# Kernel optimization log

Measured on AMD Instinct MI355X. Metric: run time of the kernel, lower is better.

Reference implementation:

```python
import jax, jax.numpy as jnp
import numpy as np
from jax import lax

WINDOW_SIZE = 11
SIGMA = 1.5
C1 = 0.01 ** 2
C2 = 0.03 ** 2
EPS_DEN = 1e-12
EPS_CLAMP = 1e-6


def _gaussian_window(size=WINDOW_SIZE, sigma=SIGMA):
    xs = jnp.arange(size, dtype=jnp.float32) - size // 2
    g = jnp.exp(-(xs ** 2) / (2.0 * sigma ** 2))
    g = g / g.sum()
    w = g[:, None] * g[None, :]
    w = w / w.sum()  # already ~1; matches torch's redundant renorm
    return w  # [k, k]


def _depthwise_filter(x, window):
    # x: [B, C, H, W]; depthwise 'SAME' conv (stride 1, odd k == pad k//2)
    ch = x.shape[1]
    k = window.shape[0]
    w = jnp.broadcast_to(window[None, None], (ch, 1, k, k)).astype(x.dtype)
    return lax.conv_general_dilated(
        x, w, window_strides=(1, 1), padding='SAME',
        feature_group_count=ch,
        dimension_numbers=('NCHW', 'OIHW', 'NCHW'))


def setup_inputs() -> dict:
    key = jax.random.key(0)
    kx, ky = jax.random.split(key)
    B, C, H, W = 32, 1, 512, 512
    x = jax.random.uniform(kx, (B, C, H, W), dtype=jnp.float32)
    y = jax.random.uniform(ky, (B, C, H, W), dtype=jnp.float32)
    return {"x": x, "y": y}


def reference(x, y):
    window = _gaussian_window().astype(x.dtype)
    mu_x = _depthwise_filter(x, window)
    mu_y = _depthwise_filter(y, window)
    sigma_x = _depthwise_filter(x * x, window) - mu_x * mu_x
    sigma_y = _depthwise_filter(y * y, window) - mu_y * mu_y
    sigma_xy = _depthwise_filter(x * y, window) - mu_x * mu_y
    num = (2.0 * mu_x * mu_y + C1) * (2.0 * sigma_xy + C2)
    den = (mu_x * mu_x + mu_y * mu_y + C1) * (sigma_x + sigma_y + C2)
    ssim_map = num / (den + EPS_DEN)
    ssim_map = jnp.clip(ssim_map, -1.0 + EPS_CLAMP, 1.0 - EPS_CLAMP)
    return 1.0 - jnp.mean(ssim_map)
```

## Files before the change

kernel.cpp:

```cpp
#include <hip/hip_runtime.h>

#define IMG    512
#define TW     32
#define TH     16
#define R      5
#define KW     11
#define HB_H   (TH + 2*R)
#define W4     33
#define W1     37
#define GX     (IMG / TW)
#define GY     (IMG / TH)
#define NBATCH 32
#define NBLOCKS (GX * GY * NBATCH)
#define NSLOTS  64
#define PERSLOT (NBLOCKS / NSLOTS)
#define C1f 0.0001f
#define C2f 0.0009f

#define SCALEF    16777216.0f
#define SSHIFT    45
#define BIAS1     (1ll << 36)
#define GSHIFT    50
#define BIAS2     (1ll << 43)

typedef float v2f __attribute__((ext_vector_type(2)));

__global__ __launch_bounds__(256, 4) void ssim_fused_kernel(
    const float* __restrict__ x, const float* __restrict__ y,
    float* __restrict__ out, unsigned long long* __restrict__ ws)
{
    __shared__ float4 hb4[HB_H][W4];
    __shared__ float  hb1[HB_H][W1];
    __shared__ float  red[4];

    const float W[KW] = {
        0.00102838f, 0.00759874f, 0.03600077f, 0.10936075f, 0.21300553f,
        0.26601172f,
        0.21300553f, 0.10936075f, 0.03600077f, 0.00759874f, 0.00102838f};

    const int tc = blockIdx.x, tr = blockIdx.y, b = blockIdx.z;
    const int tid = threadIdx.x;
    const size_t imgBase = (size_t)b * (IMG * IMG);
    const int gr0 = tr * TH - R;
    const bool colEdge = (tc == 0) || (tc == GX - 1);

    if (tid < HB_H * 8) {
        const int rr = tid >> 3;
        const int g  = tid & 7;
        const int gr = gr0 + rr;
        const bool rowok = (unsigned)gr < (unsigned)IMG;
        if (rowok) {
            const float4* rx = (const float4*)(x + imgBase + (size_t)gr * IMG);
            const float4* ry = (const float4*)(y + imgBase + (size_t)gr * IMG);
            const int c4 = tc * 8 + g - 2;
            float fx[20], fy[20];
            if (colEdge) {
#pragma unroll
                for (int i = 0; i < 5; ++i) {
                    int q = c4 + i;
                    int qc = min(max(q, 0), IMG / 4 - 1);
                    float4 vx = rx[qc], vy = ry[qc];
                    float m = (q == qc) ? 1.f : 0.f;
                    fx[4*i+0]=vx.x*m; fx[4*i+1]=vx.y*m; fx[4*i+2]=vx.z*m; fx[4*i+3]=vx.w*m;
                    fy[4*i+0]=vy.x*m; fy[4*i+1]=vy.y*m; fy[4*i+2]=vy.z*m; fy[4*i+3]=vy.w*m;
                }
            } else {
#pragma unroll
                for (int i = 0; i < 5; ++i) {
                    float4 vx = rx[c4 + i], vy = ry[c4 + i];
                    fx[4*i+0]=vx.x; fx[4*i+1]=vx.y; fx[4*i+2]=vx.z; fx[4*i+3]=vx.w;
                    fy[4*i+0]=vy.x; fy[4*i+1]=vy.y; fy[4*i+2]=vy.z; fy[4*i+3]=vy.w;
                }
            }
            v2f m[4], s[4];
            float c[4];
#pragma unroll
            for (int k = 0; k < 4; ++k) { m[k] = (v2f)(0.f); s[k] = (v2f)(0.f); c[k] = 0.f; }
#pragma unroll
            for (int j = 0; j < 14; ++j) {
                const v2f p  = { fx[3 + j], fy[3 + j] };
                const v2f pp = p * p;
                const float pq = fx[3 + j] * fy[3 + j];
#pragma unroll
                for (int k = 0; k < 4; ++k) {
                    const int u = j - k;
                    if (u >= 0 && u < KW) {
                        const float wt = W[u];
                        m[k] += wt * p;
                        s[k] += wt * pp;
                        c[k] += wt * pq;
                    }
                }
            }
#pragma unroll
            for (int k = 0; k < 4; ++k) {
                hb4[rr][4*g + k] = make_float4(m[k].x, m[k].y, s[k].x, s[k].y);
                hb1[rr][4*g + k] = c[k];
            }
        } else {
            const float4 z = make_float4(0.f, 0.f, 0.f, 0.f);
#pragma unroll
            for (int k = 0; k < 4; ++k) {
                hb4[rr][4*g + k] = z;
                hb1[rr][4*g + k] = 0.f;
            }
        }
    }
    __syncthreads();

    const int tx = tid & 31;
    const int ty = tid >> 5;
    const int r0 = ty * 2;

    v2f vm[2], vs[2];
    float vc[2];
#pragma unroll
    for (int k = 0; k < 2; ++k) { vm[k] = (v2f)(0.f); vs[k] = (v2f)(0.f); vc[k] = 0.f; }

#pragma unroll
    for (int t = 0; t < 12; ++t) {
        const float4 v4 = hb4[r0 + t][tx];
        const float  v1 = hb1[r0 + t][tx];
        const v2f a = { v4.x, v4.y };
        const v2f d = { v4.z, v4.w };
#pragma unroll
        for (int k = 0; k < 2; ++k) {
            const int u = t - k;
            if (u >= 0 && u < KW) {
                const float wt = W[u];
                vm[k] += wt * a;
                vs[k] += wt * d;
                vc[k] += wt * v1;
            }
        }
    }

    float lsum = 0.f;
#pragma unroll
    for (int k = 0; k < 2; ++k) {
        const float mux = vm[k].x, muy = vm[k].y;
        const float sxx = vs[k].x - mux * mux;
        const float syy = vs[k].y - muy * muy;
        const float sxy = vc[k]   - mux * muy;
        const float num = (2.f * mux * muy + C1f) * (2.f * sxy + C2f);
        const float den = (mux * mux + muy * muy + C1f) * (sxx + syy + C2f);
        float ssim = num / (den + 1e-12f);
        ssim = fminf(fmaxf(ssim, -1.f + 1e-6f), 1.f - 1e-6f);
        lsum += ssim;
    }

#pragma unroll
    for (int off = 32; off > 0; off >>= 1)
        lsum += __shfl_down(lsum, off, 64);
    if ((tid & 63) == 0) red[tid >> 6] = lsum;
    __syncthreads();
    if (tid == 0) {
        const float s = red[0] + red[1] + red[2] + red[3];
        const int fid  = ((b * GY) + tr) * GX + tc;
        const int slot = fid & (NSLOTS - 1);

        const long long v = (long long)llrintf(s * SCALEF);
        const unsigned long long sAdd =
            (1ull << SSHIFT) | (unsigned long long)(v + BIAS1);
        unsigned long long old = atomicAdd(&ws[16 * slot], sAdd);
        if ((old >> SSHIFT) == (unsigned long long)(PERSLOT - 1)) {
            const long long slotSum =
                (long long)((old & ((1ull << SSHIFT) - 1)) +
                            (unsigned long long)(v + BIAS1))
                - (long long)PERSLOT * BIAS1;
            const unsigned long long gAdd =
                (1ull << GSHIFT) | (unsigned long long)(slotSum + BIAS2);
            unsigned long long gold = atomicAdd(&ws[16 * NSLOTS], gAdd);
            if ((gold >> GSHIFT) == (unsigned long long)(NSLOTS - 1)) {
                const long long total =
                    (long long)((gold & ((1ull << GSHIFT) - 1)) +
                                (unsigned long long)(slotSum + BIAS2))
                    - (long long)NSLOTS * BIAS2;
                const double mean =
                    (double)total / ((double)SCALEF * (double)NBLOCKS * (double)(TW * TH));
                out[0] = (float)(1.0 - mean);
            }
        }
    }
}

extern "C" void kernel_launch(void* const* d_in, const int* in_sizes, int n_in,
                              void* d_out, int out_size, void* d_ws, size_t ws_size,
                              hipStream_t stream) {
    const float* x = (const float*)d_in[0];
    const float* y = (const float*)d_in[1];
    float* out = (float*)d_out;
    unsigned long long* ws = (unsigned long long*)d_ws;

    hipMemsetAsync(d_ws, 0, (NSLOTS + 1) * 128, stream);
    dim3 grid(GX, GY, NBATCH);
    ssim_fused_kernel<<<grid, 256, 0, stream>>>(x, y, out, ws);
}
```

Baseline: 131.1 us.

## Filter sum/difference channels and enlarge tiles to cut separable-filter work

The kernel now filters u=x+y and v=x-y and their squares, so four filtered channels replace five. The SSIM terms are rebuilt algebraically from these, which lets the separate xy shared-memory array go away. Tile height grows from 16 to 64 rows so the vertical halo overhead is amortised, and each thread now produces 8 horizontal and 8 vertical outputs with a strided column mapping. The costs are higher register pressure, fewer blocks in flight, and slightly different float rounding from the sum/difference reformulation.

```diff
diff --git a/kernel.cpp b/kernel.cpp
--- a/kernel.cpp
+++ b/kernel.cpp
@@ -2,12 +2,11 @@
 
 #define IMG    512
 #define TW     32
-#define TH     16
+#define TH     64
 #define R      5
 #define KW     11
 #define HB_H   (TH + 2*R)
 #define W4     33
-#define W1     37
 #define GX     (IMG / TW)
 #define GY     (IMG / TH)
 #define NBATCH 32
@@ -30,7 +29,6 @@
     float* __restrict__ out, unsigned long long* __restrict__ ws)
 {
     __shared__ float4 hb4[HB_H][W4];
-    __shared__ float  hb1[HB_H][W1];
     __shared__ float  red[4];
 
     const float W[KW] = {
@@ -44,107 +42,101 @@
     const int gr0 = tr * TH - R;
     const bool colEdge = (tc == 0) || (tc == GX - 1);
 
-    if (tid < HB_H * 8) {
-        const int rr = tid >> 3;
-        const int g  = tid & 7;
+    for (int i = tid; i < HB_H * 4; i += 256) {
+        const int rr = i >> 2;
+        const int g  = i & 3;
         const int gr = gr0 + rr;
-        const bool rowok = (unsigned)gr < (unsigned)IMG;
-        if (rowok) {
+        if ((unsigned)gr < (unsigned)IMG) {
             const float4* rx = (const float4*)(x + imgBase + (size_t)gr * IMG);
             const float4* ry = (const float4*)(y + imgBase + (size_t)gr * IMG);
-            const int c4 = tc * 8 + g - 2;
-            float fx[20], fy[20];
+            const int q0 = tc * 8 + 2 * g - 2;
+            float fx[24], fy[24];
             if (colEdge) {
 #pragma unroll
-                for (int i = 0; i < 5; ++i) {
-                    int q = c4 + i;
+                for (int i4 = 0; i4 < 6; ++i4) {
+                    int q = q0 + i4;
                     int qc = min(max(q, 0), IMG / 4 - 1);
                     float4 vx = rx[qc], vy = ry[qc];
                     float m = (q == qc) ? 1.f : 0.f;
-                    fx[4*i+0]=vx.x*m; fx[4*i+1]=vx.y*m; fx[4*i+2]=vx.z*m; fx[4*i+3]=vx.w*m;
-                    fy[4*i+0]=vy.x*m; fy[4*i+1]=vy.y*m; fy[4*i+2]=vy.z*m; fy[4*i+3]=vy.w*m;
+                    fx[4*i4+0]=vx.x*m; fx[4*i4+1]=vx.y*m; fx[4*i4+2]=vx.z*m; fx[4*i4+3]=vx.w*m;
+                    fy[4*i4+0]=vy.x*m; fy[4*i4+1]=vy.y*m; fy[4*i4+2]=vy.z*m; fy[4*i4+3]=vy.w*m;
                 }
             } else {
 #pragma unroll
-                for (int i = 0; i < 5; ++i) {
-                    float4 vx = rx[c4 + i], vy = ry[c4 + i];
-                    fx[4*i+0]=vx.x; fx[4*i+1]=vx.y; fx[4*i+2]=vx.z; fx[4*i+3]=vx.w;
-                    fy[4*i+0]=vy.x; fy[4*i+1]=vy.y; fy[4*i+2]=vy.z; fy[4*i+3]=vy.w;
+                for (int i4 = 0; i4 < 6; ++i4) {
+                    float4 vx = rx[q0 + i4], vy = ry[q0 + i4];
+                    fx[4*i4+0]=vx.x; fx[4*i4+1]=vx.y; fx[4*i4+2]=vx.z; fx[4*i4+3]=vx.w;
+                    fy[4*i4+0]=vy.x; fy[4*i4+1]=vy.y; fy[4*i4+2]=vy.z; fy[4*i4+3]=vy.w;
                 }
             }
-            v2f m[4], s[4];
-            float c[4];
+            v2f m[8], s[8];
 #pragma unroll
-            for (int k = 0; k < 4; ++k) { m[k] = (v2f)(0.f); s[k] = (v2f)(0.f); c[k] = 0.f; }
+            for (int k = 0; k < 8; ++k) { m[k] = (v2f)(0.f); s[k] = (v2f)(0.f); }
 #pragma unroll
-            for (int j = 0; j < 14; ++j) {
-                const v2f p  = { fx[3 + j], fy[3 + j] };
+            for (int j = 0; j < 18; ++j) {
+                const float a = fx[3 + j], c = fy[3 + j];
+                const v2f p  = { a + c, a - c };
                 const v2f pp = p * p;
-                const float pq = fx[3 + j] * fy[3 + j];
 #pragma unroll
-                for (int k = 0; k < 4; ++k) {
-                    const int u = j - k;
-                    if (u >= 0 && u < KW) {
-                        const float wt = W[u];
+                for (int k = 0; k < 8; ++k) {
+                    const int t = j - k;
+                    if (t >= 0 && t < KW) {
+                        const float wt = W[t];
                         m[k] += wt * p;
                         s[k] += wt * pp;
-                        c[k] += wt * pq;
                     }
                 }
             }
 #pragma unroll
-            for (int k = 0; k < 4; ++k) {
-                hb4[rr][4*g + k] = make_float4(m[k].x, m[k].y, s[k].x, s[k].y);
-                hb1[rr][4*g + k] = c[k];
+            for (int k = 0; k < 8; ++k) {
+                const int pos = g + 4 * k;
+                hb4[rr][pos] = make_float4(m[k].x, m[k].y, s[k].x, s[k].y);
             }
         } else {
             const float4 z = make_float4(0.f, 0.f, 0.f, 0.f);
 #pragma unroll
-            for (int k = 0; k < 4; ++k) {
-                hb4[rr][4*g + k] = z;
-                hb1[rr][4*g + k] = 0.f;
-            }
+            for (int k = 0; k < 8; ++k) hb4[rr][g + 4 * k] = z;
         }
     }
     __syncthreads();
 
-    const int tx = tid & 31;
-    const int ty = tid >> 5;
-    const int r0 = ty * 2;
+    const int tx  = tid & 31;
+    const int ty  = tid >> 5;
+    const int r0  = ty * 8;
+    const int pos = (tx >> 3) + ((tx & 7) << 2);
 
-    v2f vm[2], vs[2];
-    float vc[2];
+    v2f vm[8], vs[8];
 #pragma unroll
-    for (int k = 0; k < 2; ++k) { vm[k] = (v2f)(0.f); vs[k] = (v2f)(0.f); vc[k] = 0.f; }
+    for (int k = 0; k < 8; ++k) { vm[k] = (v2f)(0.f); vs[k] = (v2f)(0.f); }
 
 #pragma unroll
-    for (int t = 0; t < 12; ++t) {
-        const float4 v4 = hb4[r0 + t][tx];
-        const float  v1 = hb1[r0 + t][tx];
-        const v2f a = { v4.x, v4.y };
-        const v2f d = { v4.z, v4.w };
+    for (int t = 0; t < 18; ++t) {
+        const float4 h = hb4[r0 + t][pos];
+        const v2f a = { h.x, h.y };
+        const v2f d = { h.z, h.w };
 #pragma unroll
-        for (int k = 0; k < 2; ++k) {
+        for (int k = 0; k < 8; ++k) {
             const int u = t - k;
             if (u >= 0 && u < KW) {
                 const float wt = W[u];
                 vm[k] += wt * a;
                 vs[k] += wt * d;
-                vc[k] += wt * v1;
             }
         }
     }
 
     float lsum = 0.f;
 #pragma unroll
-    for (int k = 0; k < 2; ++k) {
-        const float mux = vm[k].x, muy = vm[k].y;
-        const float sxx = vs[k].x - mux * mux;
-        const float syy = vs[k].y - muy * muy;
-        const float sxy = vc[k]   - mux * muy;
-        const float num = (2.f * mux * muy + C1f) * (2.f * sxy + C2f);
-        const float den = (mux * mux + muy * muy + C1f) * (sxx + syy + C2f);
-        float ssim = num / (den + 1e-12f);
+    for (int k = 0; k < 8; ++k) {
+        const v2f sq = vm[k] * vm[k];
+        const float A = sq.x, B = sq.y;
+        const float Su = vs[k].x, Sv = vs[k].y;
+        const float AmB = A - B, ApB = A + B;
+        const float t1 = 0.5f * AmB + C1f;
+        const float t2 = 0.5f * ((Su - Sv) - AmB) + C2f;
+        const float t3 = 0.5f * ApB + C1f;
+        const float t4 = 0.5f * ((Su + Sv) - ApB) + C2f;
+        float ssim = (t1 * t2) / (t3 * t4 + 1e-12f);
         ssim = fminf(fmaxf(ssim, -1.f + 1e-6f), 1.f - 1e-6f);
         lsum += ssim;
     }
```

Result: faster. 118.1 us (-9.9%).
